# Optimization experiments

Hardware: AMD Instinct MI355X
Metric: run time of the kernel (lower is better)

The kernel has to match this reference:

```python
import jax, jax.numpy as jnp
import numpy as np

EPS = 1e-5

def layer_norm(x, g, b):
    m = jnp.mean(x, axis=-1, keepdims=True)
    v = jnp.var(x, axis=-1, keepdims=True)
    return (x - m) * jax.lax.rsqrt(v + EPS) * g + b

def setup_inputs() -> dict:
    key = jax.random.key(0)
    ks = jax.random.split(key, 10)
    A, T, c_s, c_z, c_atom, c_pair = 1024, 256, 384, 128, 128, 16
    tok = jax.random.randint(ks[0], (A,), 0, T)
    a2t = jax.nn.one_hot(tok, T, dtype=jnp.float32)  # [A, T] one-hot atom->token map
    return {
        "atom_to_token_index": a2t,
        "cl": jax.random.normal(ks[1], (A, c_atom), jnp.float32),
        "plm": jax.random.normal(ks[2], (A, A, c_pair), jnp.float32),
        "ql": jax.random.normal(ks[3], (A, c_atom), jnp.float32),
        "s_trunk": jax.random.normal(ks[4], (T, c_s), jnp.float32),
        "zij": jax.random.normal(ks[5], (T, T, c_z), jnp.float32),
        "rl": jax.random.normal(ks[6], (A, 3), jnp.float32),
        "ln_s_g": jnp.ones((c_s,), jnp.float32),
        "ln_s_b": jnp.zeros((c_s,), jnp.float32),
        "W_s": jax.random.normal(ks[7], (c_s, c_atom), jnp.float32) / np.sqrt(c_s),
        "ln_z_g": jnp.ones((c_z,), jnp.float32),
        "ln_z_b": jnp.zeros((c_z,), jnp.float32),
        "W_z": jax.random.normal(ks[8], (c_z, c_pair), jnp.float32) / np.sqrt(c_z),
        "W_r": jax.random.normal(ks[9], (3, c_atom), jnp.float32) / np.sqrt(3.0),
    }

def reference(atom_to_token_index, cl, plm, ql, s_trunk, zij, rl,
              ln_s_g, ln_s_b, W_s, ln_z_g, ln_z_b, W_z, W_r):
    a2t = atom_to_token_index  # [A, T]
    # token -> atom gather of single rep: sum_t a2t[a,t] * s_trunk[t,:]  -> [A, c_s]
    s_atom = jnp.einsum('at,tc->ac', a2t, s_trunk)
    cl = cl + layer_norm(s_atom, ln_s_g, ln_s_b) @ W_s  # [A, c_atom]
    # token-pair -> atom-pair gather: sum_{t,u} a2t[a,t] a2t[b,u] zij[t,u,:]
    # factored into two one-hot contractions (same math as the dense one-hot outer product)
    z_half = jnp.einsum('at,tuz->auz', a2t, zij)      # [A, T, c_z]
    z_atom = jnp.einsum('auz,bu->abz', z_half, a2t)    # [A, A, c_z]
    plm = plm + layer_norm(z_atom, ln_z_g, ln_z_b) @ W_z  # [A, A, c_pair]
    ql = ql + rl @ W_r  # [A, c_atom]
    return (cl, plm, ql)
```

## Files before the change

### kernel.cpp

```cpp
#include <hip/hip_runtime.h>

#define A_N 1024
#define T_N 256
#define CS 384
#define CZ 128
#define CA 128
#define CP 16
#define LN_EPS 1e-5f

typedef __bf16  bf16x8 __attribute__((ext_vector_type(8)));
typedef float   f32x4  __attribute__((ext_vector_type(4)));

#define WSTRIDE 136

__global__ __launch_bounds__(256) void token_kernel(
        const float* __restrict__ s_trunk,
        const float* __restrict__ gs,
        const float* __restrict__ bs,
        const float* __restrict__ W_s,
        float* __restrict__ Ys,
        const float* __restrict__ zij,
        const float* __restrict__ gz,
        const float* __restrict__ bz,
        const float* __restrict__ W_z,
        float* __restrict__ Yz,
        const float* __restrict__ a2t,
        int* __restrict__ tok) {
    __shared__ float xs[CS];
    __shared__ float2 sred[4];
    __shared__ float part[2][128];
    __shared__ __bf16 wb[CP * WSTRIDE];
    __shared__ float2 gb_part[16][16];
    __shared__ float Gw_sh[CP], Bw_sh[CP];

    int tid = threadIdx.x;

    if (blockIdx.x < 256) {
        int t = blockIdx.x;
        float sum = 0.f, sq = 0.f;
        {
            float v = s_trunk[t * CS + tid];
            xs[tid] = v; sum = v; sq = v * v;
            if (tid < CS - 256) {
                float v2 = s_trunk[t * CS + 256 + tid];
                xs[256 + tid] = v2; sum += v2; sq += v2 * v2;
            }
        }
        #pragma unroll
        for (int off = 32; off > 0; off >>= 1) {
            sum += __shfl_down(sum, off);
            sq  += __shfl_down(sq,  off);
        }
        if ((tid & 63) == 0) sred[tid >> 6] = make_float2(sum, sq);
        __syncthreads();
        float s_ = sred[0].x + sred[1].x + sred[2].x + sred[3].x;
        float ss = sred[0].y + sred[1].y + sred[2].y + sred[3].y;
        float m = s_ * (1.f / CS);
        float rstd = rsqrtf(ss * (1.f / CS) - m * m + LN_EPS);

        int col = tid & 127, seg = tid >> 7;
        float a0 = 0.f, a1 = 0.f, a2 = 0.f, a3 = 0.f;
        int k0 = seg * (CS / 2);
        for (int k = k0; k < k0 + CS / 2; k += 4) {
            float z0 = (xs[k + 0] - m) * rstd * gs[k + 0] + bs[k + 0];
            float z1 = (xs[k + 1] - m) * rstd * gs[k + 1] + bs[k + 1];
            float z2 = (xs[k + 2] - m) * rstd * gs[k + 2] + bs[k + 2];
            float z3 = (xs[k + 3] - m) * rstd * gs[k + 3] + bs[k + 3];
            a0 = fmaf(z0, W_s[(k + 0) * CA + col], a0);
            a1 = fmaf(z1, W_s[(k + 1) * CA + col], a1);
            a2 = fmaf(z2, W_s[(k + 2) * CA + col], a2);
            a3 = fmaf(z3, W_s[(k + 3) * CA + col], a3);
        }
        part[seg][col] = (a0 + a1) + (a2 + a3);
        __syncthreads();
        if (tid < 128) Ys[t * CA + tid] = part[0][tid] + part[1][tid];
        return;
    }

    int a = blockIdx.x - 256;

    { float v = a2t[(size_t)a * T_N + tid]; if (v > 0.5f) tok[a] = tid; }

    {
        int j = tid & 15, seg = tid >> 4;
        float sg = 0.f, sb = 0.f;
        #pragma unroll
        for (int i = 0; i < 8; ++i) {
            int k = seg * 8 + i;
            float w = W_z[k * CP + j];
            float gw = gz[k] * w;
            wb[j * WSTRIDE + k] = (__bf16)gw;
            sg += gw;
            sb = fmaf(bz[k], w, sb);
        }
        gb_part[seg][j] = make_float2(sg, sb);
    }
    __syncthreads();
    if (tid < CP) {
        float sg = 0.f, sb = 0.f;
        #pragma unroll
        for (int s = 0; s < 16; ++s) { float2 p = gb_part[s][tid]; sg += p.x; sb += p.y; }
        Gw_sh[tid] = sg; Bw_sh[tid] = sb;
    }

    int wave = tid >> 6, lane = tid & 63;
    int m    = lane & 15, quad = lane >> 4;
    size_t grow = (size_t)a * 64 + wave * 16 + m;

    const float4* zrow = (const float4*)(zij + grow * CZ);
    float4 xv[8];
    #pragma unroll
    for (int s = 0; s < 4; ++s) {
        xv[2 * s]     = zrow[quad * 2 + 8 * s];
        xv[2 * s + 1] = zrow[quad * 2 + 8 * s + 1];
    }

    float sum = 0.f, sq = 0.f;
    #pragma unroll
    for (int i = 0; i < 8; ++i) {
        float4 v = xv[i];
        sum += (v.x + v.y) + (v.z + v.w);
        sq  += v.x * v.x + v.y * v.y + v.z * v.z + v.w * v.w;
    }
    sum += __shfl_xor(sum, 16);  sq += __shfl_xor(sq, 16);
    sum += __shfl_xor(sum, 32);  sq += __shfl_xor(sq, 32);
    float mval = sum * (1.f / CZ);
    float rstd = rsqrtf(sq * (1.f / CZ) - mval * mval + LN_EPS);

    __syncthreads();

    f32x4 acc = {0.f, 0.f, 0.f, 0.f};
    #pragma unroll
    for (int s = 0; s < 4; ++s) {
        float4 v0 = xv[2 * s], v1 = xv[2 * s + 1];
        bf16x8 af;
        af[0] = (__bf16)v0.x; af[1] = (__bf16)v0.y;
        af[2] = (__bf16)v0.z; af[3] = (__bf16)v0.w;
        af[4] = (__bf16)v1.x; af[5] = (__bf16)v1.y;
        af[6] = (__bf16)v1.z; af[7] = (__bf16)v1.w;
        bf16x8 bfv = *(const bf16x8*)&wb[m * WSTRIDE + quad * 8 + 32 * s];
        acc = __builtin_amdgcn_mfma_f32_16x16x32_bf16(af, bfv, acc, 0, 0, 0);
    }

    float gwj = Gw_sh[m], bwj = Bw_sh[m];
    size_t obase = (size_t)a * 64 + wave * 16;
    #pragma unroll
    for (int i = 0; i < 4; ++i) {
        int r = quad * 4 + i;
        float mi = __shfl(mval, r);
        float ri = __shfl(rstd, r);
        float y = ri * (acc[i] - mi * gwj) + bwj;
        Yz[(obase + r) * CP + m] = y;
    }
}

__global__ __launch_bounds__(512) void atom_plm_kernel(
        const float* __restrict__ plm,
        const float* __restrict__ Yz,
        const int* __restrict__ tok,
        const float* __restrict__ cl,
        const float* __restrict__ ql,
        const float* __restrict__ rl,
        const float* __restrict__ Ys,
        const float* __restrict__ W_r,
        float* __restrict__ out_cl,
        float* __restrict__ out_plm,
        float* __restrict__ out_ql) {
    __shared__ int    tok_sh[A_N];
    __shared__ float4 yz_sh[T_N * CP / 4];

    int a = blockIdx.x;
    int tid = threadIdx.x;
    int ta = tok[a];

    if (tid < 256) ((int4*)tok_sh)[tid] = ((const int4*)tok)[tid];

    const float4* yrow = (const float4*)(Yz + (size_t)ta * (T_N * CP));
    #pragma unroll
    for (int p = 0; p < 2; ++p) {
        int j = p * 512 + tid;
        yz_sh[j ^ ((j >> 3) & 7)] = yrow[j];
    }

    if (tid < 128) {
        out_cl[a * CA + tid] = cl[a * CA + tid] + Ys[ta * CA + tid];
    } else if (tid < 256) {
        int c = tid - 128;
        float r0 = rl[a * 3 + 0], r1 = rl[a * 3 + 1], r2 = rl[a * 3 + 2];
        out_ql[a * CA + c] = ql[a * CA + c]
            + fmaf(r0, W_r[c], fmaf(r1, W_r[CA + c], r2 * W_r[2 * CA + c]));
    }
    __syncthreads();

    const float4* prow = (const float4*)(plm     + (size_t)a * (A_N * CP));
    float4*       orow = (float4*)      (out_plm + (size_t)a * (A_N * CP));
    #pragma unroll
    for (int it = 0; it < 8; ++it) {
        int f4 = it * 512 + tid;
        int b  = f4 >> 2;
        int tb = tok_sh[b];
        int x  = tb * 4 + (f4 & 3);
        float4 yv = yz_sh[x ^ ((x >> 3) & 7)];
        float4 pv = prow[f4];
        float4 o;
        o.x = pv.x + yv.x; o.y = pv.y + yv.y;
        o.z = pv.z + yv.z; o.w = pv.w + yv.w;
        orow[f4] = o;
    }
}

extern "C" void kernel_launch(void* const* d_in, const int* in_sizes, int n_in,
                              void* d_out, int out_size, void* d_ws, size_t ws_size,
                              hipStream_t stream) {
    const float* a2t     = (const float*)d_in[0];
    const float* cl      = (const float*)d_in[1];
    const float* plm     = (const float*)d_in[2];
    const float* ql      = (const float*)d_in[3];
    const float* s_trunk = (const float*)d_in[4];
    const float* zij     = (const float*)d_in[5];
    const float* rl      = (const float*)d_in[6];
    const float* ln_s_g  = (const float*)d_in[7];
    const float* ln_s_b  = (const float*)d_in[8];
    const float* W_s     = (const float*)d_in[9];
    const float* ln_z_g  = (const float*)d_in[10];
    const float* ln_z_b  = (const float*)d_in[11];
    const float* W_z     = (const float*)d_in[12];
    const float* W_r     = (const float*)d_in[13];

    int*   tok = (int*)d_ws;
    float* Ys  = (float*)((char*)d_ws + 4096);
    float* Yz  = (float*)((char*)d_ws + 4096 + 131072);

    float* out_cl  = (float*)d_out;
    float* out_plm = out_cl + A_N * CA;
    float* out_ql  = out_plm + (size_t)A_N * A_N * CP;

    token_kernel<<<256 + A_N, 256, 0, stream>>>(
        s_trunk, ln_s_g, ln_s_b, W_s, Ys,
        zij, ln_z_g, ln_z_b, W_z, Yz,
        a2t, tok);
    atom_plm_kernel<<<A_N, 512, 0, stream>>>(
        plm, Yz, tok, cl, ql, rl, Ys, W_r,
        out_cl, out_plm, out_ql);
}
```

Baseline: 182.4 us.

## Fuse token LN/projection into per-atom kernel, recomputing per atom's token

The token-level LayerNorm+projection of zij (to CP channels) and of s_trunk is moved into the per-atom plm kernel. Each atom block recomputes its token's 256x16 Yz slice directly into shared memory and its Ys row, so the Yz/Ys workspace round-trip goes away. A small separate kernel extracts token indices first. The cost is redundant recomputation: each of 1024 atom blocks rereads a 128 KB zij slice and 384x128 W_s instead of 256 token blocks doing it once, which adds heavy L2 traffic and compute.

Measured after the change: 194.8 us. 1.07x slower.

```diff
diff --git a/kernel.cpp b/kernel.cpp
--- a/kernel.cpp
+++ b/kernel.cpp
@@ -13,80 +13,58 @@
 
 #define WSTRIDE 136
 
-__global__ __launch_bounds__(256) void token_kernel(
+__global__ __launch_bounds__(256) void tok_kernel(
+        const float* __restrict__ a2t,
+        int* __restrict__ tok) {
+    int a = blockIdx.x * 4 + (threadIdx.x >> 6);
+    int lane = threadIdx.x & 63;
+    float4 v = ((const float4*)(a2t + (size_t)a * T_N))[lane];
+    if (v.x > 0.5f) tok[a] = lane * 4 + 0;
+    if (v.y > 0.5f) tok[a] = lane * 4 + 1;
+    if (v.z > 0.5f) tok[a] = lane * 4 + 2;
+    if (v.w > 0.5f) tok[a] = lane * 4 + 3;
+}
+
+__global__ __launch_bounds__(512) void fused_atom_kernel(
+        const float* __restrict__ zij,
+        const float* __restrict__ gz,
+        const float* __restrict__ bz,
+        const float* __restrict__ W_z,
+        const int* __restrict__ tok,
+        const float* __restrict__ plm,
         const float* __restrict__ s_trunk,
         const float* __restrict__ gs,
         const float* __restrict__ bs,
         const float* __restrict__ W_s,
-        float* __restrict__ Ys,
-        const float* __restrict__ zij,
-        const float* __restrict__ gz,
-        const float* __restrict__ bz,
-        const float* __restrict__ W_z,
-        float* __restrict__ Yz,
-        const float* __restrict__ a2t,
-        int* __restrict__ tok) {
-    __shared__ float xs[CS];
-    __shared__ float2 sred[4];
-    __shared__ float part[2][128];
+        const float* __restrict__ cl,
+        const float* __restrict__ ql,
+        const float* __restrict__ rl,
+        const float* __restrict__ W_r,
+        float* __restrict__ out_cl,
+        float* __restrict__ out_plm,
+        float* __restrict__ out_ql) {
     __shared__ __bf16 wb[CP * WSTRIDE];
-    __shared__ float2 gb_part[16][16];
-    __shared__ float Gw_sh[CP], Bw_sh[CP];
-
-    int tid = threadIdx.x;
-
-    if (blockIdx.x < 256) {
-        int t = blockIdx.x;
-        float sum = 0.f, sq = 0.f;
-        {
-            float v = s_trunk[t * CS + tid];
-            xs[tid] = v; sum = v; sq = v * v;
-            if (tid < CS - 256) {
-                float v2 = s_trunk[t * CS + 256 + tid];
-                xs[256 + tid] = v2; sum += v2; sq += v2 * v2;
-            }
-        }
-        #pragma unroll
-        for (int off = 32; off > 0; off >>= 1) {
-            sum += __shfl_down(sum, off);
-            sq  += __shfl_down(sq,  off);
-        }
-        if ((tid & 63) == 0) sred[tid >> 6] = make_float2(sum, sq);
-        __syncthreads();
-        float s_ = sred[0].x + sred[1].x + sred[2].x + sred[3].x;
-        float ss = sred[0].y + sred[1].y + sred[2].y + sred[3].y;
-        float m = s_ * (1.f / CS);
-        float rstd = rsqrtf(ss * (1.f / CS) - m * m + LN_EPS);
-
-        int col = tid & 127, seg = tid >> 7;
-        float a0 = 0.f, a1 = 0.f, a2 = 0.f, a3 = 0.f;
-        int k0 = seg * (CS / 2);
-        for (int k = k0; k < k0 + CS / 2; k += 4) {
-            float z0 = (xs[k + 0] - m) * rstd * gs[k + 0] + bs[k + 0];
-            float z1 = (xs[k + 1] - m) * rstd * gs[k + 1] + bs[k + 1];
-            float z2 = (xs[k + 2] - m) * rstd * gs[k + 2] + bs[k + 2];
-            float z3 = (xs[k + 3] - m) * rstd * gs[k + 3] + bs[k + 3];
-            a0 = fmaf(z0, W_s[(k + 0) * CA + col], a0);
-            a1 = fmaf(z1, W_s[(k + 1) * CA + col], a1);
-            a2 = fmaf(z2, W_s[(k + 2) * CA + col], a2);
-            a3 = fmaf(z3, W_s[(k + 3) * CA + col], a3);
-        }
-        part[seg][col] = (a0 + a1) + (a2 + a3);
-        __syncthreads();
-        if (tid < 128) Ys[t * CA + tid] = part[0][tid] + part[1][tid];
-        return;
-    }
-
-    int a = blockIdx.x - 256;
-
-    { float v = a2t[(size_t)a * T_N + tid]; if (v > 0.5f) tok[a] = tid; }
-
+    __shared__ float2 gb_part[32][16];
+    __shared__ float  Gw_sh[CP], Bw_sh[CP];
+    __shared__ int    tok_sh[A_N];
+    __shared__ float4 yz_sh[T_N * CP / 4];
+    __shared__ float  xs[CS];
+    __shared__ float2 sred[8];
+    __shared__ float  part[4][128];
+
+    int tid  = threadIdx.x;
+    int a    = blockIdx.x;
+    int wave = tid >> 6, lane = tid & 63;
+    int m16  = lane & 15, quad = lane >> 4;
+    float* yz_f = (float*)yz_sh;
+
+    if (tid < 256) ((int4*)tok_sh)[tid] = ((const int4*)tok)[tid];
     {
         int j = tid & 15, seg = tid >> 4;
         float sg = 0.f, sb = 0.f;
         #pragma unroll
-        for (int i = 0; i < 8; ++i) {
-            int k = seg * 8 + i;
+        for (int i = 0; i < 4; ++i) {
+            int k = seg * 4 + i;
             float w = W_z[k * CP + j];
             float gw = gz[k] * w;
             wb[j * WSTRIDE + k] = (__bf16)gw;
@@ -96,109 +74,116 @@
         gb_part[seg][j] = make_float2(sg, sb);
     }
     __syncthreads();
+
+    int ta = tok_sh[a];
+
     if (tid < CP) {
         float sg = 0.f, sb = 0.f;
         #pragma unroll
-        for (int s = 0; s < 16; ++s) { float2 p = gb_part[s][tid]; sg += p.x; sb += p.y; }
+        for (int s = 0; s < 32; ++s) { float2 p = gb_part[s][tid]; sg += p.x; sb += p.y; }
         Gw_sh[tid] = sg; Bw_sh[tid] = sb;
     }
 
-    int wave = tid >> 6, lane = tid & 63;
-    int m    = lane & 15, quad = lane >> 4;
-    size_t grow = (size_t)a * 64 + wave * 16 + m;
-
-    const float4* zrow = (const float4*)(zij + grow * CZ);
-    float4 xv[8];
+    float ssum = 0.f, ssq = 0.f;
+    if (tid < CS) {
+        float v = s_trunk[(size_t)ta * CS + tid];
+        xs[tid] = v; ssum = v; ssq = v * v;
+    }
     #pragma unroll
-    for (int s = 0; s < 4; ++s) {
-        xv[2 * s]     = zrow[quad * 2 + 8 * s];
-        xv[2 * s + 1] = zrow[quad * 2 + 8 * s + 1];
-    }
-
-    float sum = 0.f, sq = 0.f;
+    for (int off = 32; off > 0; off >>= 1) {
+        ssum += __shfl_down(ssum, off);
+        ssq  += __shfl_down(ssq,  off);
+    }
+    if (lane == 0) sred[wave] = make_float2(ssum, ssq);
+    __syncthreads();
+
+    const float* zbase = zij + (size_t)ta * T_N * CZ;
+    for (int s = 0; s < 2; ++s) {
+        int u = wave * 32 + s * 16 + m16;
+        const float4* zrow = (const float4*)(zbase + (size_t)u * CZ);
+        float4 xv[8];
+        #pragma unroll
+        for (int kk = 0; kk < 4; ++kk) {
+            xv[2 * kk]     = zrow[quad * 2 + 8 * kk];
+            xv[2 * kk + 1] = zrow[quad * 2 + 8 * kk + 1];
+        }
+        float zsum = 0.f, zsq = 0.f;
+        #pragma unroll
+        for (int i = 0; i < 8; ++i) {
+            float4 v = xv[i];
+            zsum += (v.x + v.y) + (v.z + v.w);
+            zsq  += v.x * v.x + v.y * v.y + v.z * v.z + v.w * v.w;
+        }
+        zsum += __shfl_xor(zsum, 16);  zsq += __shfl_xor(zsq, 16);
+        zsum += __shfl_xor(zsum, 32);  zsq += __shfl_xor(zsq, 32);
+        float mval = zsum * (1.f / CZ);
+        float rstd = rsqrtf(zsq * (1.f / CZ) - mval * mval + LN_EPS);
+
+        f32x4 acc = {0.f, 0.f, 0.f, 0.f};
+        #pragma unroll
+        for (int kk = 0; kk < 4; ++kk) {
+            float4 v0 = xv[2 * kk], v1 = xv[2 * kk + 1];
+            bf16x8 af;
+            af[0] = (__bf16)v0.x; af[1] = (__bf16)v0.y;
+            af[2] = (__bf16)v0.z; af[3] = (__bf16)v0.w;
+            af[4] = (__bf16)v1.x; af[5] = (__bf16)v1.y;
+            af[6] = (__bf16)v1.z; af[7] = (__bf16)v1.w;
+            bf16x8 bfv = *(const bf16x8*)&wb[m16 * WSTRIDE + quad * 8 + 32 * kk];
+            acc = __builtin_amdgcn_mfma_f32_16x16x32_bf16(af, bfv, acc, 0, 0, 0);
+        }
+
+        float gwj = Gw_sh[m16], bwj = Bw_sh[m16];
+        #pragma unroll
+        for (int i = 0; i < 4; ++i) {
+            int r  = quad * 4 + i;
+            int uu = wave * 32 + s * 16 + r;
+            float mi = __shfl(mval, r);
+            float ri = __shfl(rstd, r);
+            float y  = ri * (acc[i] - mi * gwj) + bwj;
+            int x4 = uu * 4 + (m16 >> 2);
+            yz_f[(x4 ^ ((x4 >> 3) & 7)) * 4 + (m16 & 3)] = y;
+        }
+    }
+
+    float s_ = 0.f, ss = 0.f;
     #pragma unroll
-    for (int i = 0; i < 8; ++i) {
-        float4 v = xv[i];
-        sum += (v.x + v.y) + (v.z + v.w);
-        sq  += v.x * v.x + v.y * v.y + v.z * v.z + v.w * v.w;
-    }
-    sum += __shfl_xor(sum, 16);  sq += __shfl_xor(sq, 16);
-    sum += __shfl_xor(sum, 32);  sq += __shfl_xor(sq, 32);
-    float mval = sum * (1.f / CZ);
-    float rstd = rsqrtf(sq * (1.f / CZ) - mval * mval + LN_EPS);
-
+    for (int i = 0; i < 8; ++i) { s_ += sred[i].x; ss += sred[i].y; }
+    float mS = s_ * (1.f / CS);
+    float rS = rsqrtf(ss * (1.f / CS) - mS * mS + LN_EPS);
+    {
+        int col = tid & 127, segk = tid >> 7;
+        float a0 = 0.f, a1 = 0.f, a2 = 0.f, a3 = 0.f;
+        int k0 = segk * (CS / 4);
+        for (int k = k0; k < k0 + CS / 4; k += 4) {
+            float z0 = (xs[k + 0] - mS) * rS * gs[k + 0] + bs[k + 0];
+            float z1 = (xs[k + 1] - mS) * rS * gs[k + 1] + bs[k + 1];
+            float z2 = (xs[k + 2] - mS) * rS * gs[k + 2] + bs[k + 2];
+            float z3 = (xs[k + 3] - mS) * rS * gs[k + 3] + bs[k + 3];
+            a0 = fmaf(z0, W_s[(k + 0) * CA + col], a0);
+            a1 = fmaf(z1, W_s[(k + 1) * CA + col], a1);
+            a2 = fmaf(z2, W_s[(k + 2) * CA + col], a2);
+            a3 = fmaf(z3, W_s[(k + 3) * CA + col], a3);
+        }
+        part[segk][col] = (a0 + a1) + (a2 + a3);
+    }
     __syncthreads();
 
-    f32x4 acc = {0.f, 0.f, 0.f, 0.f};
-    #pragma unroll
-    for (int s = 0; s < 4; ++s) {
-        float4 v0 = xv[2 * s], v1 = xv[2 * s + 1];
-        bf16x8 af;
-        af[0] = (__bf16)v0.x; af[1] = (__bf16)v0.y;
-        af[2] = (__bf16)v0.z; af[3] = (__bf16)v0.w;
-        af[4] = (__bf16)v1.x; af[5] = (__bf16)v1.y;
-        af[6] = (__bf16)v1.z; af[7] = (__bf16)v1.w;
-        bf16x8 bfv = *(const bf16x8*)&wb[m * WSTRIDE + quad * 8 + 32 * s];
-        acc = __builtin_amdgcn_mfma_f32_16x16x32_bf16(af, bfv, acc, 0, 0, 0);
-    }
-
-    float gwj = Gw_sh[m], bwj = Bw_sh[m];
-    size_t obase = (size_t)a * 64 + wave * 16;
-    #pragma unroll
-    for (int i = 0; i < 4; ++i) {
-        int r = quad * 4 + i;
-        float mi = __shfl(mval, r);
-        float ri = __shfl(rstd, r);
-        float y = ri * (acc[i] - mi * gwj) + bwj;
-        Yz[(obase + r) * CP + m] = y;
-    }
-}
-
-__global__ __launch_bounds__(512) void atom_plm_kernel(
-        const float* __restrict__ plm,
-        const float* __restrict__ Yz,
-        const int* __restrict__ tok,
-        const float* __restrict__ cl,
-        const float* __restrict__ ql,
-        const float* __restrict__ rl,
-        const float* __restrict__ Ys,
-        const float* __restrict__ W_r,
-        float* __restrict__ out_cl,
-        float* __restrict__ out_plm,
-        float* __restrict__ out_ql) {
-    __shared__ int    tok_sh[A_N];
-    __shared__ float4 yz_sh[T_N * CP / 4];
-
-    int a = blockIdx.x;
-    int tid = threadIdx.x;
-    int ta = tok[a];
-
-    if (tid < 256) ((int4*)tok_sh)[tid] = ((const int4*)tok)[tid];
-
-    const float4* yrow = (const float4*)(Yz + (size_t)ta * (T_N * CP));
-    #pragma unroll
-    for (int p = 0; p < 2; ++p) {
-        int j = p * 512 + tid;
-        yz_sh[j ^ ((j >> 3) & 7)] = yrow[j];
-    }
-
     if (tid < 128) {
-        out_cl[a * CA + tid] = cl[a * CA + tid] + Ys[ta * CA + tid];
+        out_cl[(size_t)a * CA + tid] = cl[(size_t)a * CA + tid]
+            + ((part[0][tid] + part[1][tid]) + (part[2][tid] + part[3][tid]));
     } else if (tid < 256) {
         int c = tid - 128;
         float r0 = rl[a * 3 + 0], r1 = rl[a * 3 + 1], r2 = rl[a * 3 + 2];
-        out_ql[a * CA + c] = ql[a * CA + c]
+        out_ql[(size_t)a * CA + c] = ql[(size_t)a * CA + c]
             + fmaf(r0, W_r[c], fmaf(r1, W_r[CA + c], r2 * W_r[2 * CA + c]));
     }
-    __syncthreads();
 
     const float4* prow = (const float4*)(plm     + (size_t)a * (A_N * CP));
     float4*       orow = (float4*)      (out_plm + (size_t)a * (A_N * CP));
     #pragma unroll
     for (int it = 0; it < 8; ++it) {
         int f4 = it * 512 + tid;
-        int b  = f4 >> 2;
-        int tb = tok_sh[b];
+        int tb = tok_sh[f4 >> 2];
         int x  = tb * 4 + (f4 & 3);
         float4 yv = yz_sh[x ^ ((x >> 3) & 7)];
         float4 pv = prow[f4];
@@ -227,19 +212,16 @@
     const float* W_z     = (const float*)d_in[12];
     const float* W_r     = (const float*)d_in[13];
 
-    int*   tok = (int*)d_ws;
-    float* Ys  = (float*)((char*)d_ws + 4096);
-    float* Yz  = (float*)((char*)d_ws + 4096 + 131072);
+    int* tok = (int*)d_ws;
 
     float* out_cl  = (float*)d_out;
     float* out_plm = out_cl + A_N * CA;
     float* out_ql  = out_plm + (size_t)A_N * A_N * CP;
 
-    token_kernel<<<256 + A_N, 256, 0, stream>>>(
-        s_trunk, ln_s_g, ln_s_b, W_s, Ys,
-        zij, ln_z_g, ln_z_b, W_z, Yz,
-        a2t, tok);
-    atom_plm_kernel<<<A_N, 512, 0, stream>>>(
-        plm, Yz, tok, cl, ql, rl, Ys, W_r,
+    tok_kernel<<<T_N, 256, 0, stream>>>(a2t, tok);
+    fused_atom_kernel<<<A_N, 512, 0, stream>>>(
+        zij, ln_z_g, ln_z_b, W_z, tok,
+        plm, s_trunk, ln_s_g, ln_s_b, W_s,
+        cl, ql, rl, W_r,
         out_cl, out_plm, out_ql);
 }
```
